# Kernel optimization log

Hardware: AMD Instinct MI355X
Metric: run time of the kernel (lower is better)

Reference implementation:

```python
import jax, jax.numpy as jnp
import numpy as np

B, N, D = 2, 2048, 1024
H, DH = 16, 64
DI = 4096
EPS = 1e-5
NEG_SLOPE = 0.01  # F.leaky_relu default


def _ln(x, g, b):
    mu = jnp.mean(x, axis=-1, keepdims=True)
    var = jnp.mean((x - mu) ** 2, axis=-1, keepdims=True)
    return (x - mu) * jax.lax.rsqrt(var + EPS) * g + b


def setup_inputs() -> dict:
    key = jax.random.key(0)
    ks = jax.random.split(key, 10)
    s = 0.02
    return {
        "Z": jax.random.normal(ks[0], (B, N, D), jnp.float32),
        "new_mask": jax.random.normal(ks[1], (B, N, N), jnp.float32),
        "mask": jax.random.uniform(ks[2], (B, N, N), jnp.float32),
        "ln1_g": jnp.ones((D,), jnp.float32),
        "ln1_b": jnp.zeros((D,), jnp.float32),
        "qkv_w": jax.random.normal(ks[3], (3 * D, D), jnp.float32) * s,
        "qkv_b": jnp.zeros((3 * D,), jnp.float32),
        "o_w": jax.random.normal(ks[4], (D, H * DH), jnp.float32) * s,
        "ln2_g": jnp.ones((D,), jnp.float32),
        "ln2_b": jnp.zeros((D,), jnp.float32),
        "p1_w": jax.random.normal(ks[5], (DI, D), jnp.float32) * s,
        "p1_b": jnp.zeros((DI,), jnp.float32),
        "p2_w": jax.random.normal(ks[6], (D, DI), jnp.float32) * s,
        "p2_b": jnp.zeros((D,), jnp.float32),
    }


def reference(Z, new_mask, mask, ln1_g, ln1_b, qkv_w, qkv_b, o_w, ln2_g, ln2_b, p1_w, p1_b, p2_w, p2_b):
    inp = Z
    Zn = _ln(Z, ln1_g, ln1_b)
    qkv = (Zn @ qkv_w.T + qkv_b).reshape(B, N, H, 3 * DH)
    # torch chunk order in the source: V, Q, K
    V, Q, K = jnp.split(qkv, 3, axis=3)  # each [B,N,H,DH]
    # scores: einsum('bnij,bmij->binm') == [B,H,N,N]
    W = jnp.einsum("bnhd,bmhd->bhnm", Q, K) / np.sqrt(DH) + new_mask[:, None]
    A = jax.nn.softmax(W, axis=3) * mask[:, None]
    attn = jnp.einsum("bhnm,bmhd->bnhd", A, V).reshape(B, N, D)
    attn = jnp.where(attn >= 0, attn, NEG_SLOPE * attn) @ o_w.T  # leaky_relu then o_net (no bias)
    Z1 = attn + inp
    Zn2 = _ln(Z1, ln2_g, ln2_b)
    h = jax.nn.relu(Zn2 @ p1_w.T + p1_b)
    return h @ p2_w.T + p2_b + Z1
```

## Files before the change

kernel.cpp:

```cpp
#include <hip/hip_runtime.h>

typedef unsigned short u16;
typedef __attribute__((ext_vector_type(8))) short bf16x8;
typedef __attribute__((ext_vector_type(4))) float f32x4;

#define DEV static __device__ __forceinline__

DEV u16 f2bf(float f) {
    unsigned u = __float_as_uint(f);
    u += 0x7FFFu + ((u >> 16) & 1u);
    return (u16)(u >> 16);
}

typedef const __attribute__((address_space(1))) void* gas1_t;
typedef __attribute__((address_space(3))) void* gas3_t;

DEV void gl_lds16(const u16* g, u16* l) {
    __builtin_amdgcn_global_load_lds((gas1_t)g, (gas3_t)l, 16, 0, 0);
}

DEV int sw8(int row, int chunk) { return row * 64 + ((chunk ^ (row & 7)) << 3); }

__global__ void cast_bf16(const float* __restrict__ in, u16* __restrict__ out, int n4) {
    int i = blockIdx.x * blockDim.x + threadIdx.x;
    if (i < n4) {
        float4 v = ((const float4*)in)[i];
        ushort4 o;
        o.x = f2bf(v.x); o.y = f2bf(v.y); o.z = f2bf(v.z); o.w = f2bf(v.w);
        ((ushort4*)out)[i] = o;
    }
}

__global__ void cast_qkv(const float* __restrict__ in, u16* __restrict__ out) {
    int i = blockIdx.x * 256 + threadIdx.x;
    int orow = i >> 8, cc = i & 255;
    int region = orow >> 10, rem = orow & 1023, h = rem >> 6, t = rem & 63;
    int srow = h * 192 + region * 64 + t;
    float4 v = ((const float4*)in)[srow * 256 + cc];
    ushort4 o;
    o.x = f2bf(v.x); o.y = f2bf(v.y); o.z = f2bf(v.z); o.w = f2bf(v.w);
    ((ushort4*)out)[i] = o;
}

__global__ void permute_bias(const float* __restrict__ in, float* __restrict__ out) {
    int i = blockIdx.x * 256 + threadIdx.x;
    if (i < 3072) {
        int region = i >> 10, rem = i & 1023, h = rem >> 6, t = rem & 63;
        out[i] = in[h * 192 + region * 64 + t];
    }
}

__global__ void pack_mask(const float* __restrict__ nm, const float* __restrict__ pm,
                          unsigned* __restrict__ out, int n4) {
    int i = blockIdx.x * blockDim.x + threadIdx.x;
    if (i < n4) {
        float4 a = ((const float4*)nm)[i];
        float4 b = ((const float4*)pm)[i];
        uint4 o;
        o.x = ((unsigned)f2bf(b.x) << 16) | f2bf(a.x * 1.4426950f);
        o.y = ((unsigned)f2bf(b.y) << 16) | f2bf(a.y * 1.4426950f);
        o.z = ((unsigned)f2bf(b.z) << 16) | f2bf(a.z * 1.4426950f);
        o.w = ((unsigned)f2bf(b.w) << 16) | f2bf(a.w * 1.4426950f);
        ((uint4*)out)[i] = o;
    }
}

__global__ __launch_bounds__(256) void ln_bf16(const float* __restrict__ x,
                                               const float* __restrict__ gam,
                                               const float* __restrict__ bet,
                                               u16* __restrict__ y) {
    const int row = blockIdx.x;
    const int t = threadIdx.x;
    const float4 v = ((const float4*)(x + (size_t)row * 1024))[t];
    float s = v.x + v.y + v.z + v.w;
    float ss = v.x * v.x + v.y * v.y + v.z * v.z + v.w * v.w;
#pragma unroll
    for (int o = 1; o < 64; o <<= 1) {
        s += __shfl_xor(s, o);
        ss += __shfl_xor(ss, o);
    }
    __shared__ float rs[4], rss[4];
    const int wave = t >> 6, lane = t & 63;
    if (lane == 0) { rs[wave] = s; rss[wave] = ss; }
    __syncthreads();
    const float tot = rs[0] + rs[1] + rs[2] + rs[3];
    const float totss = rss[0] + rss[1] + rss[2] + rss[3];
    const float mu = tot * (1.0f / 1024.0f);
    const float var = totss * (1.0f / 1024.0f) - mu * mu;
    const float rstd = rsqrtf(var + 1e-5f);
    const float4 g4 = ((const float4*)gam)[t];
    const float4 b4 = ((const float4*)bet)[t];
    ushort4 o;
    o.x = f2bf((v.x - mu) * rstd * g4.x + b4.x);
    o.y = f2bf((v.y - mu) * rstd * g4.y + b4.y);
    o.z = f2bf((v.z - mu) * rstd * g4.z + b4.z);
    o.w = f2bf((v.w - mu) * rstd * g4.w + b4.w);
    ((ushort4*)(y + (size_t)row * 1024))[t] = o;
}

template <int EPI>
__global__ __launch_bounds__(256, 2) void gemm_bt(const u16* __restrict__ A,
                                                  const u16* __restrict__ Bt,
                                                  const float* __restrict__ bias,
                                                  const float* __restrict__ res,
                                                  void* __restrict__ out0,
                                                  void* __restrict__ out1,
                                                  void* __restrict__ out2,
                                                  int M, int N, int K) {
    __shared__ __align__(16) u16 As[128 * 32];
    __shared__ __align__(16) u16 Bs[128 * 32];
    const int tid = threadIdx.x;
    const int wave = tid >> 6, lane = tid & 63;
    const int lhi = lane >> 4, llo = lane & 15;
    const int bx = blockIdx.x, by = blockIdx.y;

    const int arow = wave * 32 + (lane >> 2);
    const int acol = (lane & 3) * 8;
    const u16* gA = A + (size_t)(by * 128 + arow) * K + acol;
    const u16* gB = Bt + (size_t)(bx * 128 + arow) * K + acol;
    u16* lA = As + wave * 1024 + lane * 8;
    u16* lB = Bs + wave * 1024 + lane * 8;

    const int wr = wave >> 1, wc = wave & 1;
    const f32x4 zero = {0.f, 0.f, 0.f, 0.f};
    f32x4 acc[4][4];
#pragma unroll
    for (int i = 0; i < 4; i++)
#pragma unroll
        for (int j = 0; j < 4; j++) acc[i][j] = zero;

    for (int k0 = 0; k0 < K; k0 += 32) {
        __syncthreads();
        gl_lds16(gA, lA);
        gl_lds16(gA + 16 * (size_t)K, lA + 512);
        gl_lds16(gB, lB);
        gl_lds16(gB + 16 * (size_t)K, lB + 512);
        gA += 32; gB += 32;
        __syncthreads();
        bf16x8 af[4], bfr[4];
#pragma unroll
        for (int i = 0; i < 4; i++)
            af[i] = *(const bf16x8*)(As + (wr * 64 + i * 16 + llo) * 32 + lhi * 8);
#pragma unroll
        for (int j = 0; j < 4; j++)
            bfr[j] = *(const bf16x8*)(Bs + (wc * 64 + j * 16 + llo) * 32 + lhi * 8);
#pragma unroll
        for (int i = 0; i < 4; i++)
#pragma unroll
            for (int j = 0; j < 4; j++)
                acc[i][j] = __builtin_amdgcn_mfma_f32_16x16x32_bf16(af[i], bfr[j], acc[i][j], 0, 0, 0);
    }

    const int rbase = by * 128 + wr * 64 + lhi * 4;
    const int cbase = bx * 128 + wc * 64 + llo;
#pragma unroll
    for (int i = 0; i < 4; i++) {
#pragma unroll
        for (int j = 0; j < 4; j++) {
#pragma unroll
            for (int r = 0; r < 4; r++) {
                const int row = rbase + i * 16 + r;
                const int col = cbase + j * 16;
                float v = acc[i][j][r];
                if (EPI == 0) {
                    v += bias[col];
                    const int region = col >> 10;
                    const int c = col & 1023;
                    const int b = row >> 11, n = row & 2047;
                    if (region == 0) {
                        ((float*)out0)[(size_t)row * 1024 + c] = v;
                    } else {
                        const int h = c >> 6, t = c & 63;
                        u16* dst = (region == 1) ? (u16*)out1 : (u16*)out2;
                        dst[(((size_t)(b * 16 + h)) * 2048 + n) * 64 + t] = f2bf(v);
                    }
                } else if (EPI == 1) {
                    ((float*)out0)[(size_t)row * N + col] = v + res[(size_t)row * N + col];
                } else if (EPI == 2) {
                    v += bias[col];
                    v = v > 0.f ? v : 0.f;
                    ((u16*)out0)[(size_t)row * N + col] = f2bf(v);
                } else {
                    v += bias[col] + res[(size_t)row * N + col];
                    ((float*)out0)[(size_t)row * N + col] = v;
                }
            }
        }
    }
}

__global__ __launch_bounds__(256) void vtrans(const float* __restrict__ Vsc,
                                              u16* __restrict__ Vt) {
    __shared__ u16 Ts[64 * 72];
    const int nt = blockIdx.x;
    const int bh = blockIdx.y;
    const int b = bh >> 4, h = bh & 15;
    const int t = threadIdx.x;
    const int n0 = nt * 64;
    const int nr = t >> 2;
    const int dq = (t & 3) * 16;
    const float* src = Vsc + ((size_t)(b * 2048 + n0 + nr)) * 1024 + h * 64 + dq;
    float4 v0 = ((const float4*)src)[0];
    float4 v1 = ((const float4*)src)[1];
    float4 v2 = ((const float4*)src)[2];
    float4 v3 = ((const float4*)src)[3];
    u16* c0 = Ts + nr;
    c0[(dq + 0) * 72]  = f2bf(v0.x); c0[(dq + 1) * 72]  = f2bf(v0.y);
    c0[(dq + 2) * 72]  = f2bf(v0.z); c0[(dq + 3) * 72]  = f2bf(v0.w);
    c0[(dq + 4) * 72]  = f2bf(v1.x); c0[(dq + 5) * 72]  = f2bf(v1.y);
    c0[(dq + 6) * 72]  = f2bf(v1.z); c0[(dq + 7) * 72]  = f2bf(v1.w);
    c0[(dq + 8) * 72]  = f2bf(v2.x); c0[(dq + 9) * 72]  = f2bf(v2.y);
    c0[(dq + 10) * 72] = f2bf(v2.z); c0[(dq + 11) * 72] = f2bf(v2.w);
    c0[(dq + 12) * 72] = f2bf(v3.x); c0[(dq + 13) * 72] = f2bf(v3.y);
    c0[(dq + 14) * 72] = f2bf(v3.z); c0[(dq + 15) * 72] = f2bf(v3.w);
    __syncthreads();
    const int d = t >> 2, n8 = (t & 3) * 16;
    bf16x8 o0 = *(const bf16x8*)(Ts + d * 72 + n8);
    bf16x8 o1 = *(const bf16x8*)(Ts + d * 72 + n8 + 8);
    u16* dst = Vt + ((size_t)bh * 64 + d) * 2048 + n0 + n8;
    *(bf16x8*)dst = o0;
    *(bf16x8*)(dst + 8) = o1;
}

__global__ __launch_bounds__(256, 2) void attn_fused2(const u16* __restrict__ Qg,
                                                      const u16* __restrict__ Kg,
                                                      const u16* __restrict__ Vt,
                                                      const unsigned* __restrict__ Mp,
                                                      u16* __restrict__ attnL) {
    __shared__ __align__(16) u16 Qs[128 * 64];
    __shared__ __align__(16) u16 Ks[64 * 64];
    __shared__ __align__(16) u16 Vs[64 * 64];
    __shared__ __align__(16) u16 Ps[128 * 64];
    const int tid = threadIdx.x, wave = tid >> 6, lane = tid & 63;
    const int lhi = lane >> 4, llo = lane & 15;
    const int id = blockIdx.x;
    const int hh = id >> 5, bq = id & 31;
    const int b = bq >> 4, qt = bq & 15;
    const int bh = b * 16 + hh;
    const int q0 = qt * 128;
    const int l3 = lane >> 3, l7 = lane & 7;
    const int swcol = (l7 ^ (l3 & 7)) * 8;

#pragma unroll
    for (int s = 0; s < 4; s++) {
        const int row = wave * 32 + s * 8 + l3;
        gl_lds16(Qg + ((size_t)bh * 2048 + q0 + row) * 64 + swcol,
                 Qs + wave * 2048 + s * 512 + lane * 8);
    }

    const unsigned* Mpb = Mp + (size_t)b * 2048 * 2048;
    int midx[2][4];
#pragma unroll
    for (int i = 0; i < 2; i++)
#pragma unroll
        for (int r = 0; r < 4; r++)
            midx[i][r] = (q0 + wave * 32 + i * 16 + lhi * 4 + r) * 2048 + llo;

    const f32x4 zero = {0.f, 0.f, 0.f, 0.f};
    f32x4 accO[2][4];
    float lsum[2][4];
#pragma unroll
    for (int i = 0; i < 2; i++)
#pragma unroll
        for (int j = 0; j < 4; j++) accO[i][j] = zero;
#pragma unroll
    for (int i = 0; i < 2; i++)
#pragma unroll
        for (int r = 0; r < 4; r++) lsum[i][r] = 0.f;

    const float CS = 0.125f * 1.4426950f;

    for (int m0 = 0; m0 < 2048; m0 += 64) {
        __syncthreads();
#pragma unroll
        for (int s = 0; s < 2; s++) {
            const int row = wave * 16 + s * 8 + l3;
            gl_lds16(Kg + ((size_t)bh * 2048 + m0 + row) * 64 + swcol,
                     Ks + wave * 1024 + s * 512 + lane * 8);
            gl_lds16(Vt + ((size_t)bh * 64 + row) * 2048 + m0 + swcol,
                     Vs + wave * 1024 + s * 512 + lane * 8);
        }
        unsigned mv[2][4][4];
#pragma unroll
        for (int i = 0; i < 2; i++)
#pragma unroll
            for (int r = 0; r < 4; r++)
#pragma unroll
                for (int j = 0; j < 4; j++)
                    mv[i][r][j] = Mpb[midx[i][r] + m0 + j * 16];
        __syncthreads();

        f32x4 sacc[2][4];
#pragma unroll
        for (int i = 0; i < 2; i++)
#pragma unroll
            for (int j = 0; j < 4; j++) sacc[i][j] = zero;
#pragma unroll
        for (int kk = 0; kk < 2; kk++) {
            bf16x8 aq[2];
#pragma unroll
            for (int i = 0; i < 2; i++)
                aq[i] = *(const bf16x8*)(Qs + sw8(wave * 32 + i * 16 + llo, kk * 4 + lhi));
#pragma unroll
            for (int j = 0; j < 4; j++) {
                const bf16x8 bk = *(const bf16x8*)(Ks + sw8(j * 16 + llo, kk * 4 + lhi));
                sacc[0][j] = __builtin_amdgcn_mfma_f32_16x16x32_bf16(aq[0], bk, sacc[0][j], 0, 0, 0);
                sacc[1][j] = __builtin_amdgcn_mfma_f32_16x16x32_bf16(aq[1], bk, sacc[1][j], 0, 0, 0);
            }
        }

#pragma unroll
        for (int i = 0; i < 2; i++)
#pragma unroll
            for (int j = 0; j < 4; j++)
#pragma unroll
                for (int r = 0; r < 4; r++) {
                    const unsigned u = mv[i][r][j];
                    const float nm = __uint_as_float(u << 16);
                    const float pm = __uint_as_float(u & 0xFFFF0000u);
                    const float e = exp2f(fmaf(sacc[i][j][r], CS, nm));
                    lsum[i][r] += e;
                    const float p = e * pm;
                    const u16 pb = (u16)((__float_as_uint(p) + 0x8000u) >> 16);
                    const int q_rel = wave * 32 + i * 16 + lhi * 4 + r;
                    const int ch = (j * 2 + (llo >> 3)) ^ (q_rel & 7);
                    Ps[q_rel * 64 + ch * 8 + (llo & 7)] = pb;
                }

#pragma unroll
        for (int kk = 0; kk < 2; kk++) {
            bf16x8 ap[2];
#pragma unroll
            for (int i = 0; i < 2; i++)
                ap[i] = *(const bf16x8*)(Ps + sw8(wave * 32 + i * 16 + llo, kk * 4 + lhi));
#pragma unroll
            for (int jd = 0; jd < 4; jd++) {
                const bf16x8 bv = *(const bf16x8*)(Vs + sw8(jd * 16 + llo, kk * 4 + lhi));
                accO[0][jd] = __builtin_amdgcn_mfma_f32_16x16x32_bf16(ap[0], bv, accO[0][jd], 0, 0, 0);
                accO[1][jd] = __builtin_amdgcn_mfma_f32_16x16x32_bf16(ap[1], bv, accO[1][jd], 0, 0, 0);
            }
        }
    }

#pragma unroll
    for (int i = 0; i < 2; i++)
#pragma unroll
        for (int r = 0; r < 4; r++) {
#pragma unroll
            for (int o = 1; o < 16; o <<= 1) lsum[i][r] += __shfl_xor(lsum[i][r], o);
            lsum[i][r] = 1.0f / lsum[i][r];
        }
#pragma unroll
    for (int i = 0; i < 2; i++)
#pragma unroll
        for (int jd = 0; jd < 4; jd++)
#pragma unroll
            for (int r = 0; r < 4; r++) {
                float v = accO[i][jd][r] * lsum[i][r];
                v = v >= 0.f ? v : 0.01f * v;
                const int q = q0 + wave * 32 + i * 16 + lhi * 4 + r;
                attnL[((size_t)b * 2048 + q) * 1024 + hh * 64 + jd * 16 + llo] = f2bf(v);
            }
}

extern "C" void kernel_launch(void* const* d_in, const int* in_sizes, int n_in,
                              void* d_out, int out_size, void* d_ws, size_t ws_size,
                              hipStream_t stream) {
    const float* Z     = (const float*)d_in[0];
    const float* nmask = (const float*)d_in[1];
    const float* pmask = (const float*)d_in[2];
    const float* ln1_g = (const float*)d_in[3];
    const float* ln1_b = (const float*)d_in[4];
    const float* qkv_w = (const float*)d_in[5];
    const float* qkv_b = (const float*)d_in[6];
    const float* o_w   = (const float*)d_in[7];
    const float* ln2_g = (const float*)d_in[8];
    const float* ln2_b = (const float*)d_in[9];
    const float* p1_w  = (const float*)d_in[10];
    const float* p1_b  = (const float*)d_in[11];
    const float* p2_w  = (const float*)d_in[12];
    const float* p2_b  = (const float*)d_in[13];
    float* out = (float*)d_out;

    char* w = (char*)d_ws;
    auto take = [&](size_t bytes) -> char* {
        char* p = w;
        w += (bytes + 255) & ~(size_t)255;
        return p;
    };
    u16* qkvW   = (u16*)take((size_t)3072 * 1024 * 2);
    u16* oW     = (u16*)take((size_t)1024 * 1024 * 2);
    u16* p1W    = (u16*)take((size_t)4096 * 1024 * 2);
    u16* p2W    = (u16*)take((size_t)1024 * 4096 * 2);
    u16* Zn     = (u16*)take((size_t)4096 * 1024 * 2);
    u16* Qb     = (u16*)take((size_t)32 * 2048 * 64 * 2);
    u16* Kb     = (u16*)take((size_t)32 * 2048 * 64 * 2);
    u16* Vt     = (u16*)take((size_t)32 * 64 * 2048 * 2);
    u16* attnL  = (u16*)take((size_t)4096 * 1024 * 2);
    float* Z1   = (float*)take((size_t)4096 * 1024 * 4);
    u16* hbuf   = (u16*)take((size_t)4096 * 4096 * 2);
    unsigned* Mp = (unsigned*)take((size_t)2 * 2048 * 2048 * 4);
    float* pbias = (float*)take((size_t)3072 * 4);
    float* Vsc   = (float*)hbuf;

    cast_qkv<<<dim3(3072), 256, 0, stream>>>(qkv_w, qkvW);
    permute_bias<<<dim3(12), 256, 0, stream>>>(qkv_b, pbias);
    cast_bf16<<<dim3(1024), 256, 0, stream>>>(o_w, oW, 1024 * 1024 / 4);
    cast_bf16<<<dim3(4096), 256, 0, stream>>>(p1_w, p1W, 4096 * 1024 / 4);
    cast_bf16<<<dim3(4096), 256, 0, stream>>>(p2_w, p2W, 1024 * 4096 / 4);
    pack_mask<<<dim3(8192), 256, 0, stream>>>(nmask, pmask, Mp, 2 * 2048 * 2048 / 4);

    ln_bf16<<<dim3(4096), 256, 0, stream>>>(Z, ln1_g, ln1_b, Zn);
    gemm_bt<0><<<dim3(24, 32), 256, 0, stream>>>(Zn, qkvW, pbias, nullptr, Vsc, Qb, Kb, 4096, 3072, 1024);
    vtrans<<<dim3(32, 32), 256, 0, stream>>>(Vsc, Vt);
    attn_fused2<<<dim3(512), 256, 0, stream>>>(Qb, Kb, Vt, Mp, attnL);
    gemm_bt<1><<<dim3(8, 32), 256, 0, stream>>>(attnL, oW, nullptr, Z, Z1, nullptr, nullptr, 4096, 1024, 1024);
    ln_bf16<<<dim3(4096), 256, 0, stream>>>(Z1, ln2_g, ln2_b, Zn);
    gemm_bt<2><<<dim3(32, 32), 256, 0, stream>>>(Zn, p1W, p1_b, nullptr, hbuf, nullptr, nullptr, 4096, 4096, 1024);
    gemm_bt<3><<<dim3(8, 32), 256, 0, stream>>>(hbuf, p2W, p2_b, Z1, out, nullptr, nullptr, 4096, 1024, 4096);
}
```

Baseline: 476.3 us.

## Add 128x64 GEMM tiles for N=1024 GEMMs and prefetch mask in attention

The GEMM kernel gains a BN template parameter. The two N=1024 GEMMs (o_net and p2) now use 128x64 tiles, which doubles their grid from 256 to 512 blocks to fill more CUs. The attention kernel now prefetches the next tile's packed mask values into registers by ping-ponging between two register sets. It also replaces the XOR-swizzled P buffer with a row stride padded to 72, which simplifies the store addressing. The trade-offs are extra register pressure from the double-buffered mask and lower MFMA reuse per block in the smaller GEMM tiles.

Result: no change. 475.2 us (-0.2%).

```diff
diff --git a/kernel.cpp b/kernel.cpp
--- a/kernel.cpp
+++ b/kernel.cpp
@@ -98,7 +98,7 @@
     ((ushort4*)(y + (size_t)row * 1024))[t] = o;
 }
 
-template <int EPI>
+template <int EPI, int BN>
 __global__ __launch_bounds__(256, 2) void gemm_bt(const u16* __restrict__ A,
                                                   const u16* __restrict__ Bt,
                                                   const float* __restrict__ bias,
@@ -107,25 +107,28 @@
                                                   void* __restrict__ out1,
                                                   void* __restrict__ out2,
                                                   int M, int N, int K) {
+    constexpr int RT = (BN == 128) ? 4 : 2;
     __shared__ __align__(16) u16 As[128 * 32];
-    __shared__ __align__(16) u16 Bs[128 * 32];
+    __shared__ __align__(16) u16 Bs[BN * 32];
     const int tid = threadIdx.x;
     const int wave = tid >> 6, lane = tid & 63;
     const int lhi = lane >> 4, llo = lane & 15;
     const int bx = blockIdx.x, by = blockIdx.y;
+    const int wr = (BN == 128) ? (wave >> 1) : wave;
+    const int wc = (BN == 128) ? (wave & 1) : 0;
 
     const int arow = wave * 32 + (lane >> 2);
     const int acol = (lane & 3) * 8;
     const u16* gA = A + (size_t)(by * 128 + arow) * K + acol;
-    const u16* gB = Bt + (size_t)(bx * 128 + arow) * K + acol;
     u16* lA = As + wave * 1024 + lane * 8;
-    u16* lB = Bs + wave * 1024 + lane * 8;
-
-    const int wr = wave >> 1, wc = wave & 1;
+    const int brow = (BN == 128) ? arow : (wave * 16 + (lane >> 2));
+    const u16* gB = Bt + (size_t)(bx * BN + brow) * K + acol;
+    u16* lB = Bs + ((BN == 128) ? wave * 1024 : wave * 512) + lane * 8;
+
     const f32x4 zero = {0.f, 0.f, 0.f, 0.f};
-    f32x4 acc[4][4];
-#pragma unroll
-    for (int i = 0; i < 4; i++)
+    f32x4 acc[RT][4];
+#pragma unroll
+    for (int i = 0; i < RT; i++)
 #pragma unroll
         for (int j = 0; j < 4; j++) acc[i][j] = zero;
 
@@ -134,27 +137,27 @@
         gl_lds16(gA, lA);
         gl_lds16(gA + 16 * (size_t)K, lA + 512);
         gl_lds16(gB, lB);
-        gl_lds16(gB + 16 * (size_t)K, lB + 512);
+        if (BN == 128) gl_lds16(gB + 16 * (size_t)K, lB + 512);
         gA += 32; gB += 32;
         __syncthreads();
-        bf16x8 af[4], bfr[4];
-#pragma unroll
-        for (int i = 0; i < 4; i++)
-            af[i] = *(const bf16x8*)(As + (wr * 64 + i * 16 + llo) * 32 + lhi * 8);
+        bf16x8 af[RT], bfr[4];
+#pragma unroll
+        for (int i = 0; i < RT; i++)
+            af[i] = *(const bf16x8*)(As + (wr * (RT * 16) + i * 16 + llo) * 32 + lhi * 8);
 #pragma unroll
         for (int j = 0; j < 4; j++)
             bfr[j] = *(const bf16x8*)(Bs + (wc * 64 + j * 16 + llo) * 32 + lhi * 8);
 #pragma unroll
-        for (int i = 0; i < 4; i++)
+        for (int i = 0; i < RT; i++)
 #pragma unroll
             for (int j = 0; j < 4; j++)
                 acc[i][j] = __builtin_amdgcn_mfma_f32_16x16x32_bf16(af[i], bfr[j], acc[i][j], 0, 0, 0);
     }
 
-    const int rbase = by * 128 + wr * 64 + lhi * 4;
-    const int cbase = bx * 128 + wc * 64 + llo;
-#pragma unroll
-    for (int i = 0; i < 4; i++) {
+    const int rbase = by * 128 + wr * (RT * 16) + lhi * 4;
+    const int cbase = bx * BN + wc * 64 + llo;
+#pragma unroll
+    for (int i = 0; i < RT; i++) {
 #pragma unroll
         for (int j = 0; j < 4; j++) {
 #pragma unroll
@@ -162,7 +165,7 @@
                 const int row = rbase + i * 16 + r;
                 const int col = cbase + j * 16;
                 float v = acc[i][j][r];
-                if (EPI == 0) {
+                if constexpr (EPI == 0) {
                     v += bias[col];
                     const int region = col >> 10;
                     const int c = col & 1023;
@@ -174,9 +177,9 @@
                         u16* dst = (region == 1) ? (u16*)out1 : (u16*)out2;
                         dst[(((size_t)(b * 16 + h)) * 2048 + n) * 64 + t] = f2bf(v);
                     }
-                } else if (EPI == 1) {
+                } else if constexpr (EPI == 1) {
                     ((float*)out0)[(size_t)row * N + col] = v + res[(size_t)row * N + col];
-                } else if (EPI == 2) {
+                } else if constexpr (EPI == 2) {
                     v += bias[col];
                     v = v > 0.f ? v : 0.f;
                     ((u16*)out0)[(size_t)row * N + col] = f2bf(v);
@@ -222,7 +225,7 @@
     *(bf16x8*)(dst + 8) = o1;
 }
 
-__global__ __launch_bounds__(256, 2) void attn_fused2(const u16* __restrict__ Qg,
+__global__ __launch_bounds__(256, 2) void attn_fused3(const u16* __restrict__ Qg,
                                                       const u16* __restrict__ Kg,
                                                       const u16* __restrict__ Vt,
                                                       const unsigned* __restrict__ Mp,
@@ -230,7 +233,7 @@
     __shared__ __align__(16) u16 Qs[128 * 64];
     __shared__ __align__(16) u16 Ks[64 * 64];
     __shared__ __align__(16) u16 Vs[64 * 64];
-    __shared__ __align__(16) u16 Ps[128 * 64];
+    __shared__ __align__(16) u16 Ps[128 * 72];
     const int tid = threadIdx.x, wave = tid >> 6, lane = tid & 63;
     const int lhi = lane >> 4, llo = lane & 15;
     const int id = blockIdx.x;
@@ -270,7 +273,15 @@
 
     const float CS = 0.125f * 1.4426950f;
 
-    for (int m0 = 0; m0 < 2048; m0 += 64) {
+    unsigned mvA[2][4][4], mvB[2][4][4];
+#pragma unroll
+    for (int i = 0; i < 2; i++)
+#pragma unroll
+        for (int r = 0; r < 4; r++)
+#pragma unroll
+            for (int j = 0; j < 4; j++) mvA[i][r][j] = Mpb[midx[i][r] + j * 16];
+
+    auto body = [&](int m0, unsigned (&cur)[2][4][4], unsigned (&nxt)[2][4][4]) {
         __syncthreads();
 #pragma unroll
         for (int s = 0; s < 2; s++) {
@@ -280,15 +291,15 @@
             gl_lds16(Vt + ((size_t)bh * 64 + row) * 2048 + m0 + swcol,
                      Vs + wave * 1024 + s * 512 + lane * 8);
         }
-        unsigned mv[2][4][4];
+        __syncthreads();
+
+        const int mn = (m0 + 64) & 2047;
 #pragma unroll
         for (int i = 0; i < 2; i++)
 #pragma unroll
             for (int r = 0; r < 4; r++)
 #pragma unroll
-                for (int j = 0; j < 4; j++)
-                    mv[i][r][j] = Mpb[midx[i][r] + m0 + j * 16];
-        __syncthreads();
+                for (int j = 0; j < 4; j++) nxt[i][r][j] = Mpb[midx[i][r] + mn + j * 16];
 
         f32x4 sacc[2][4];
 #pragma unroll
@@ -310,29 +321,28 @@
         }
 
 #pragma unroll
-        for (int i = 0; i < 2; i++)
+        for (int i = 0; i < 2; i++) {
+            const int pb0 = (wave * 32 + i * 16 + lhi * 4) * 72 + llo;
 #pragma unroll
             for (int j = 0; j < 4; j++)
 #pragma unroll
                 for (int r = 0; r < 4; r++) {
-                    const unsigned u = mv[i][r][j];
+                    const unsigned u = cur[i][r][j];
                     const float nm = __uint_as_float(u << 16);
                     const float pm = __uint_as_float(u & 0xFFFF0000u);
                     const float e = exp2f(fmaf(sacc[i][j][r], CS, nm));
                     lsum[i][r] += e;
                     const float p = e * pm;
-                    const u16 pb = (u16)((__float_as_uint(p) + 0x8000u) >> 16);
-                    const int q_rel = wave * 32 + i * 16 + lhi * 4 + r;
-                    const int ch = (j * 2 + (llo >> 3)) ^ (q_rel & 7);
-                    Ps[q_rel * 64 + ch * 8 + (llo & 7)] = pb;
+                    Ps[pb0 + r * 72 + j * 16] = (u16)((__float_as_uint(p) + 0x8000u) >> 16);
                 }
+        }
 
 #pragma unroll
         for (int kk = 0; kk < 2; kk++) {
             bf16x8 ap[2];
 #pragma unroll
             for (int i = 0; i < 2; i++)
-                ap[i] = *(const bf16x8*)(Ps + sw8(wave * 32 + i * 16 + llo, kk * 4 + lhi));
+                ap[i] = *(const bf16x8*)(Ps + (wave * 32 + i * 16 + llo) * 72 + kk * 32 + lhi * 8);
 #pragma unroll
             for (int jd = 0; jd < 4; jd++) {
                 const bf16x8 bv = *(const bf16x8*)(Vs + sw8(jd * 16 + llo, kk * 4 + lhi));
@@ -340,6 +350,11 @@
                 accO[1][jd] = __builtin_amdgcn_mfma_f32_16x16x32_bf16(ap[1], bv, accO[1][jd], 0, 0, 0);
             }
         }
+    };
+
+    for (int m0 = 0; m0 < 2048; m0 += 128) {
+        body(m0, mvA, mvB);
+        body(m0 + 64, mvB, mvA);
     }
 
 #pragma unroll
@@ -411,11 +426,11 @@
     pack_mask<<<dim3(8192), 256, 0, stream>>>(nmask, pmask, Mp, 2 * 2048 * 2048 / 4);
 
     ln_bf16<<<dim3(4096), 256, 0, stream>>>(Z, ln1_g, ln1_b, Zn);
-    gemm_bt<0><<<dim3(24, 32), 256, 0, stream>>>(Zn, qkvW, pbias, nullptr, Vsc, Qb, Kb, 4096, 3072, 1024);
+    gemm_bt<0, 128><<<dim3(24, 32), 256, 0, stream>>>(Zn, qkvW, pbias, nullptr, Vsc, Qb, Kb, 4096, 3072, 1024);
     vtrans<<<dim3(32, 32), 256, 0, stream>>>(Vsc, Vt);
-    attn_fused2<<<dim3(512), 256, 0, stream>>>(Qb, Kb, Vt, Mp, attnL);
-    gemm_bt<1><<<dim3(8, 32), 256, 0, stream>>>(attnL, oW, nullptr, Z, Z1, nullptr, nullptr, 4096, 1024, 1024);
+    attn_fused3<<<dim3(512), 256, 0, stream>>>(Qb, Kb, Vt, Mp, attnL);
+    gemm_bt<1, 64><<<dim3(16, 32), 256, 0, stream>>>(attnL, oW, nullptr, Z, Z1, nullptr, nullptr, 4096, 1024, 1024);
     ln_bf16<<<dim3(4096), 256, 0, stream>>>(Z1, ln2_g, ln2_b, Zn);
-    gemm_bt<2><<<dim3(32, 32), 256, 0, stream>>>(Zn, p1W, p1_b, nullptr, hbuf, nullptr, nullptr, 4096, 4096, 1024);
-    gemm_bt<3><<<dim3(8, 32), 256, 0, stream>>>(hbuf, p2W, p2_b, Z1, out, nullptr, nullptr, 4096, 1024, 4096);
-}
+    gemm_bt<2, 128><<<dim3(32, 32), 256, 0, stream>>>(Zn, p1W, p1_b, nullptr, hbuf, nullptr, nullptr, 4096, 4096, 1024);
+    gemm_bt<3, 64><<<dim3(16, 32), 256, 0, stream>>>(hbuf, p2W, p2_b, Z1, out, nullptr, nullptr, 4096, 1024, 4096);
+}
```
